# Kernel tuning notes

Measured on AMD Instinct MI355X. Metric: run time of the kernel, lower is better.

Reference implementation:

```python
import jax, jax.numpy as jnp
import numpy as np

WINDOW_3D = (5, 11, 11)
SIGMA_3D = (0.7, 1.5, 1.5)
VALUE_MAGNITUDE = 1.0
USE_GAUSSIAN = True
CHANNEL = 1


def _gaussian(n, sigma):
    x = np.arange(n, dtype=np.float64)
    g = np.exp(-((x - n // 2) ** 2) / (2.0 * sigma ** 2))
    return g / g.sum()


def _make_window():
    if USE_GAUSSIAN:
        wz = _gaussian(WINDOW_3D[0], SIGMA_3D[0])
        wy = _gaussian(WINDOW_3D[1], SIGMA_3D[1])
        wx = _gaussian(WINDOW_3D[2], SIGMA_3D[2])
    else:
        wz = np.full(WINDOW_3D[0], 1.0 / WINDOW_3D[0])
        wy = np.full(WINDOW_3D[1], 1.0 / WINDOW_3D[1])
        wx = np.full(WINDOW_3D[2], 1.0 / WINDOW_3D[2])
    win = np.einsum('z,y,x->zyx', wz, wy, wx).astype(np.float32)
    # depthwise kernel: (C, 1, wz, wy, wx)
    return jnp.asarray(np.broadcast_to(win, (CHANNEL, 1) + WINDOW_3D).copy())


def _dwconv3d(x, w):
    pad = [(s // 2, s // 2) for s in WINDOW_3D]
    return jax.lax.conv_general_dilated(
        x, w, window_strides=(1, 1, 1), padding=pad,
        dimension_numbers=('NCDHW', 'OIDHW', 'NCDHW'),
        feature_group_count=CHANNEL)


def setup_inputs() -> dict:
    key = jax.random.key(0)
    k1, k2 = jax.random.split(key)
    shape = (8, 1, 32, 256, 256)
    img1 = jax.random.uniform(k1, shape, dtype=jnp.float32)
    img2 = jax.random.uniform(k2, shape, dtype=jnp.float32)
    return {"img1": img1, "img2": img2}


def reference(img1, img2):
    w = _make_window().astype(img1.dtype)
    mu1 = _dwconv3d(img1, w)
    mu2 = _dwconv3d(img2, w)
    mu1_sq = mu1 * mu1
    mu2_sq = mu2 * mu2
    mu1_mu2 = mu1 * mu2
    sigma1_sq = _dwconv3d(img1 * img1, w) - mu1_sq
    sigma2_sq = _dwconv3d(img2 * img2, w) - mu2_sq
    sigma12 = _dwconv3d(img1 * img2, w) - mu1_mu2
    C1 = (VALUE_MAGNITUDE * 0.01) ** 2
    C2 = (VALUE_MAGNITUDE * 0.03) ** 2
    ssim_map = ((2 * mu1_mu2 + C1) * (2 * sigma12 + C2)) / (
        (mu1_sq + mu2_sq + C1) * (sigma1_sq + sigma2_sq + C2))
    ssim = jnp.mean(ssim_map, axis=(0, 2, 3, 4))  # per-channel mean
    return 1.0 - ssim
```

## Files before the change

kernel.cpp:

```cpp
#include <hip/hip_runtime.h>
#include <hip/hip_fp16.h>
#include <math.h>


typedef __attribute__((ext_vector_type(2))) float f32x2;

#define DEPTH   32
#define HEIGHT  256
#define WIDTH   256
#define HW      (HEIGHT*WIDTH)
#define COUNT   16777216.0
#define NACC    64

#define PDW   22
#define PROWS 44
#define PLSZ  (PROWS*PDW)

struct Weights { float wz[5]; float wy[11]; };

__device__ __forceinline__ f32x2 fma2(f32x2 a, f32x2 b, f32x2 c) {
  return __builtin_elementwise_fma(a, b, c);
}
__device__ __forceinline__ f32x2 bc2(float v) { f32x2 r; r.x = v; r.y = v; return r; }

__global__ __launch_bounds__(256, 4) void ssim3d_h16b(
    const float* __restrict__ img1, const float* __restrict__ img2,
    double* __restrict__ acc, Weights W)
{
  __shared__ __align__(16) __half2 PL[5 * PLSZ];
  __shared__ float wred[4];
  const int tid = threadIdx.x;

  int bid = blockIdx.x;
  bid = (bid & 7) * 2048 + (bid >> 3);
  const int txi = bid & 7, tyi = (bid >> 3) & 7, z_out = (bid >> 6) & 31, n = bid >> 11;
  const int x0 = txi * 32 - 6;
  const int y0 = tyi * 32 - 5;

  const int cp = tid % 22, g = tid / 22;
  f32x2 zacc[4][5];
#pragma unroll
  for (int i = 0; i < 4; ++i)
#pragma unroll
    for (int f = 0; f < 5; ++f) zacc[i][f] = bc2(0.f);

  if (g < 11) {
    const int gx0 = x0 + 2 * cp;
    if ((unsigned)gx0 <= 254u) {
      const size_t nbase = (size_t)n * DEPTH * HW;
      int rofs[4];
#pragma unroll
      for (int i = 0; i < 4; ++i) {
        int gy = y0 + 4 * g + i;
        rofs[i] = min(max(gy, 0), 255) * WIDTH;
      }
#pragma unroll
      for (int kz = 0; kz < 5; ++kz) {
        int z_in = z_out + kz - 2;
        if ((unsigned)z_in >= 32u) continue;
        const f32x2 wz2 = bc2(W.wz[kz]);
        const float* p1 = img1 + nbase + (size_t)z_in * HW + gx0;
        const float* p2 = img2 + nbase + (size_t)z_in * HW + gx0;
#pragma unroll
        for (int i = 0; i < 4; ++i) {
          f32x2 A = *(const f32x2*)(p1 + rofs[i]);
          f32x2 B = *(const f32x2*)(p2 + rofs[i]);
          f32x2 t = wz2 * A, u = wz2 * B;
          zacc[i][0] += t;
          zacc[i][1] += u;
          zacc[i][2] = fma2(t, A, zacc[i][2]);
          zacc[i][3] = fma2(u, B, zacc[i][3]);
          zacc[i][4] = fma2(t, B, zacc[i][4]);
        }
      }
    }
#pragma unroll
    for (int i = 0; i < 4; ++i) {
      int row = 4 * g + i;
#pragma unroll
      for (int f = 0; f < 5; ++f)
        PL[f * PLSZ + row * PDW + cp] =
            __float22half2_rn(make_float2(zacc[i][f].x, zacc[i][f].y));
    }
  }
  __syncthreads();

  __half2 wy2[11];
#pragma unroll
  for (int j = 0; j < 11; ++j) wy2[j] = __float2half2_rn(W.wy[j]);

  const int g2 = tid / 22, xp = tid % 22;
  const bool act3 = (g2 < 11);
  const bool yedge = (tyi == 0) || (tyi == 7);
#pragma unroll
  for (int f = 0; f < 5; ++f) {
    __half2 yout[3];
    if (act3) {
      const __half2* pf = PL + f * PLSZ + xp;
      __half2 win[13];
#pragma unroll
      for (int i = 0; i < 13; ++i) win[i] = pf[(3 * g2 + i) * PDW];
      if (yedge) {
#pragma unroll
        for (int i = 0; i < 13; ++i)
          if ((unsigned)(y0 + 3 * g2 + i) >= 256u) win[i] = __float2half2_rn(0.f);
      }
#pragma unroll
      for (int r = 0; r < 3; ++r) {
        __half2 s = __float2half2_rn(0.f);
#pragma unroll
        for (int j = 0; j < 11; ++j) s = __hfma2(wy2[j], win[r + j], s);
        yout[r] = s;
      }
    }
    __syncthreads();
    if (act3) {
#pragma unroll
      for (int r = 0; r < 3; ++r) {
        int y = 3 * g2 + r;
        if (y < 32) PL[f * PLSZ + y * PDW + xp] = yout[r];
      }
    }
  }
  __syncthreads();

  const int yy = tid & 31;
  const int xh = tid >> 5;
  float sf[5][4];
#pragma unroll
  for (int f = 0; f < 5; ++f) {
    const uint2* pp = (const uint2*)(PL + f * PLSZ + yy * PDW + xh * 2);
    uint2 d0 = pp[0], d1 = pp[1], d2 = pp[2], d3 = pp[3];
    unsigned dw[8] = {d0.x, d0.y, d1.x, d1.y, d2.x, d2.y, d3.x, d3.y};
    float w[16];
#pragma unroll
    for (int m = 0; m < 8; ++m) {
      float2 fp = __half22float2(*(__half2*)&dw[m]);
      w[2 * m] = fp.x; w[2 * m + 1] = fp.y;
    }
#pragma unroll
    for (int k = 0; k < 4; ++k) {
      float sv = 0.f;
#pragma unroll
      for (int j = 0; j < 11; ++j)
        sv = fmaf(W.wy[j], w[k + 1 + j], sv);
      sf[f][k] = sv;
    }
  }

  float lsum = 0.f;
  const float C1 = 1e-4f, C2 = 9e-4f;
#pragma unroll
  for (int k = 0; k < 4; ++k) {
    float mu1 = sf[0][k], mu2 = sf[1][k];
    float m11 = mu1 * mu1, m22 = mu2 * mu2, m12 = mu1 * mu2;
    float s1 = sf[2][k] - m11, s2 = sf[3][k] - m22, s12 = sf[4][k] - m12;
    float num = fmaf(2.f, m12, C1) * fmaf(2.f, s12, C2);
    float den = (m11 + m22 + C1) * (s1 + s2 + C2);
#if __has_builtin(__builtin_amdgcn_rcpf)
    lsum = fmaf(num, __builtin_amdgcn_rcpf(den), lsum);
#else
    lsum += num / den;
#endif
  }

#pragma unroll
  for (int off = 32; off > 0; off >>= 1) lsum += __shfl_down(lsum, off, 64);
  if ((tid & 63) == 0) wred[tid >> 6] = lsum;
  __syncthreads();
  if (tid == 0) {
    float bs = wred[0] + wred[1] + wred[2] + wred[3];
    atomicAdd(&acc[blockIdx.x & (NACC - 1)], (double)bs);
  }
}

__global__ void ssim3d_finalize(const double* __restrict__ acc, float* __restrict__ out)
{
  double s = 0.0;
  for (int i = 0; i < NACC; ++i) s += acc[i];
  out[0] = 1.0f - (float)(s / COUNT);
}

static Weights make_weights()
{
  Weights W;
  double gbuf[11]; double s;

  s = 0.0;
  for (int i = 0; i < 5; ++i) {
    double d = i - 2;
    gbuf[i] = exp(-(d * d) / (2.0 * 0.7 * 0.7));
    s += gbuf[i];
  }
  for (int i = 0; i < 5; ++i) W.wz[i] = (float)(gbuf[i] / s);

  s = 0.0;
  for (int i = 0; i < 11; ++i) {
    double d = i - 5;
    gbuf[i] = exp(-(d * d) / (2.0 * 1.5 * 1.5));
    s += gbuf[i];
  }
  for (int i = 0; i < 11; ++i) W.wy[i] = (float)(gbuf[i] / s);

  return W;
}

extern "C" void kernel_launch(void* const* d_in, const int* in_sizes, int n_in,
                              void* d_out, int out_size, void* d_ws, size_t ws_size,
                              hipStream_t stream)
{
  const float* img1 = (const float*)d_in[0];
  const float* img2 = (const float*)d_in[1];
  float* out = (float*)d_out;
  double* acc = (double*)d_ws;

  hipMemsetAsync(d_ws, 0, NACC * sizeof(double), stream);

  Weights W = make_weights();

  const int n_blocks = 8 * DEPTH * 8 * 8;
  ssim3d_h16b<<<dim3(n_blocks), dim3(256), 0, stream>>>(img1, img2, acc, W);
  ssim3d_finalize<<<1, 1, 0, stream>>>(acc, out);
}
```

Baseline: 131.4 us.

## Move z-pass and final x-pass to packed fp16 with compile-time weights

Converts inputs to fp16 right after loading and runs the z-direction accumulation with packed half FMAs instead of fp32. The final horizontal pass uses pair-packed fp16 weights, applying packed FMAs over the half2 data and summing the two lanes. Weights become compile-time constants, and launch bounds move from 4 to 6 blocks per SM for more occupancy. Doing more of the pipeline in fp16 cuts ALU work and register use, but raises rounding error, notably in the variance terms computed from squared half values.

```diff
diff --git a/kernel.cpp b/kernel.cpp
--- a/kernel.cpp
+++ b/kernel.cpp
@@ -1,9 +1,8 @@
 #include <hip/hip_runtime.h>
-#include <hip/hip_fp16.h>
-#include <math.h>
 
 
 typedef __attribute__((ext_vector_type(2))) float f32x2;
+typedef _Float16 h2 __attribute__((ext_vector_type(2)));
 
 #define DEPTH   32
 #define HEIGHT  256
@@ -13,23 +12,49 @@
 #define NACC    64
 
 #define PDW   22
-#define PROWS 44
-#define PLSZ  (PROWS*PDW)
-
-struct Weights { float wz[5]; float wy[11]; };
-
-__device__ __forceinline__ f32x2 fma2(f32x2 a, f32x2 b, f32x2 c) {
+#define PLSZ  (44*PDW)
+
+#define W0h 0x1436u
+#define W1h 0x1FC8u
+#define W2h 0x289Cu
+#define W3h 0x2F00u
+#define W4h 0x32D1u
+#define W5h 0x3442u
+
+__device__ __forceinline__ h2 h2bits(unsigned u) {
+  h2 r; __builtin_memcpy(&r, &u, 4); return r;
+}
+__device__ __forceinline__ h2 hfma2v(h2 a, h2 b, h2 c) {
   return __builtin_elementwise_fma(a, b, c);
 }
-__device__ __forceinline__ f32x2 bc2(float v) { f32x2 r; r.x = v; r.y = v; return r; }
-
-__global__ __launch_bounds__(256, 4) void ssim3d_h16b(
+__device__ __forceinline__ h2 pkrtz(float x, float y) {
+#if __has_builtin(__builtin_amdgcn_cvt_pkrtz)
+  auto t = __builtin_amdgcn_cvt_pkrtz(x, y);
+  h2 r; __builtin_memcpy(&r, &t, 4); return r;
+#else
+  h2 r; r.x = (_Float16)x; r.y = (_Float16)y; return r;
+#endif
+}
+
+__global__ __launch_bounds__(256, 6) void ssim3d_h16c(
     const float* __restrict__ img1, const float* __restrict__ img2,
-    double* __restrict__ acc, Weights W)
+    double* __restrict__ acc)
 {
-  __shared__ __align__(16) __half2 PL[5 * PLSZ];
+  __shared__ __align__(16) h2 PL[5 * PLSZ];
   __shared__ float wred[4];
   const int tid = threadIdx.x;
+
+  constexpr unsigned WYB[11] = {
+    W0h|(W0h<<16), W1h|(W1h<<16), W2h|(W2h<<16), W3h|(W3h<<16), W4h|(W4h<<16),
+    W5h|(W5h<<16),
+    W4h|(W4h<<16), W3h|(W3h<<16), W2h|(W2h<<16), W1h|(W1h<<16), W0h|(W0h<<16)};
+  constexpr unsigned WZB[5] = {
+    0x20ED20EDu, 0x32933293u, 0x388F388Fu, 0x32933293u, 0x20ED20EDu};
+  constexpr unsigned WP[4][8] = {
+    {0x14360000u, 0x289C1FC8u, 0x32D12F00u, 0x32D13442u, 0x289C2F00u, 0x14361FC8u, 0u, 0u},
+    {0u, 0x1FC81436u, 0x2F00289Cu, 0x344232D1u, 0x2F0032D1u, 0x1FC8289Cu, 0x00001436u, 0u},
+    {0u, 0x14360000u, 0x289C1FC8u, 0x32D12F00u, 0x32D13442u, 0x289C2F00u, 0x14361FC8u, 0u},
+    {0u, 0u, 0x1FC81436u, 0x2F00289Cu, 0x344232D1u, 0x2F0032D1u, 0x1FC8289Cu, 0x00001436u}};
 
   int bid = blockIdx.x;
   bid = (bid & 7) * 2048 + (bid >> 3);
@@ -38,11 +63,11 @@
   const int y0 = tyi * 32 - 5;
 
   const int cp = tid % 22, g = tid / 22;
-  f32x2 zacc[4][5];
+  h2 zacc[4][5];
 #pragma unroll
   for (int i = 0; i < 4; ++i)
 #pragma unroll
-    for (int f = 0; f < 5; ++f) zacc[i][f] = bc2(0.f);
+    for (int f = 0; f < 5; ++f) zacc[i][f] = (h2){(_Float16)0, (_Float16)0};
 
   if (g < 11) {
     const int gx0 = x0 + 2 * cp;
@@ -58,19 +83,19 @@
       for (int kz = 0; kz < 5; ++kz) {
         int z_in = z_out + kz - 2;
         if ((unsigned)z_in >= 32u) continue;
-        const f32x2 wz2 = bc2(W.wz[kz]);
+        const h2 wzh = h2bits(WZB[kz]);
         const float* p1 = img1 + nbase + (size_t)z_in * HW + gx0;
         const float* p2 = img2 + nbase + (size_t)z_in * HW + gx0;
 #pragma unroll
         for (int i = 0; i < 4; ++i) {
           f32x2 A = *(const f32x2*)(p1 + rofs[i]);
           f32x2 B = *(const f32x2*)(p2 + rofs[i]);
-          f32x2 t = wz2 * A, u = wz2 * B;
-          zacc[i][0] += t;
-          zacc[i][1] += u;
-          zacc[i][2] = fma2(t, A, zacc[i][2]);
-          zacc[i][3] = fma2(u, B, zacc[i][3]);
-          zacc[i][4] = fma2(t, B, zacc[i][4]);
+          h2 ah = pkrtz(A.x, A.y), bh = pkrtz(B.x, B.y);
+          zacc[i][0] = hfma2v(wzh, ah, zacc[i][0]);
+          zacc[i][1] = hfma2v(wzh, bh, zacc[i][1]);
+          zacc[i][2] = hfma2v(wzh, ah * ah, zacc[i][2]);
+          zacc[i][3] = hfma2v(wzh, bh * bh, zacc[i][3]);
+          zacc[i][4] = hfma2v(wzh, ah * bh, zacc[i][4]);
         }
       }
     }
@@ -79,37 +104,33 @@
       int row = 4 * g + i;
 #pragma unroll
       for (int f = 0; f < 5; ++f)
-        PL[f * PLSZ + row * PDW + cp] =
-            __float22half2_rn(make_float2(zacc[i][f].x, zacc[i][f].y));
+        PL[f * PLSZ + row * PDW + cp] = zacc[i][f];
     }
   }
   __syncthreads();
-
-  __half2 wy2[11];
-#pragma unroll
-  for (int j = 0; j < 11; ++j) wy2[j] = __float2half2_rn(W.wy[j]);
 
   const int g2 = tid / 22, xp = tid % 22;
   const bool act3 = (g2 < 11);
   const bool yedge = (tyi == 0) || (tyi == 7);
 #pragma unroll
   for (int f = 0; f < 5; ++f) {
-    __half2 yout[3];
+    h2 yout[3];
     if (act3) {
-      const __half2* pf = PL + f * PLSZ + xp;
-      __half2 win[13];
+      const h2* pf = PL + f * PLSZ + xp;
+      h2 win[13];
 #pragma unroll
       for (int i = 0; i < 13; ++i) win[i] = pf[(3 * g2 + i) * PDW];
       if (yedge) {
 #pragma unroll
         for (int i = 0; i < 13; ++i)
-          if ((unsigned)(y0 + 3 * g2 + i) >= 256u) win[i] = __float2half2_rn(0.f);
+          if ((unsigned)(y0 + 3 * g2 + i) >= 256u)
+            win[i] = (h2){(_Float16)0, (_Float16)0};
       }
 #pragma unroll
       for (int r = 0; r < 3; ++r) {
-        __half2 s = __float2half2_rn(0.f);
-#pragma unroll
-        for (int j = 0; j < 11; ++j) s = __hfma2(wy2[j], win[r + j], s);
+        h2 s = (h2){(_Float16)0, (_Float16)0};
+#pragma unroll
+        for (int j = 0; j < 11; ++j) s = hfma2v(h2bits(WYB[j]), win[r + j], s);
         yout[r] = s;
       }
     }
@@ -129,22 +150,17 @@
   float sf[5][4];
 #pragma unroll
   for (int f = 0; f < 5; ++f) {
-    const uint2* pp = (const uint2*)(PL + f * PLSZ + yy * PDW + xh * 2);
-    uint2 d0 = pp[0], d1 = pp[1], d2 = pp[2], d3 = pp[3];
-    unsigned dw[8] = {d0.x, d0.y, d1.x, d1.y, d2.x, d2.y, d3.x, d3.y};
-    float w[16];
-#pragma unroll
-    for (int m = 0; m < 8; ++m) {
-      float2 fp = __half22float2(*(__half2*)&dw[m]);
-      w[2 * m] = fp.x; w[2 * m + 1] = fp.y;
-    }
+    const h2* pp = PL + f * PLSZ + yy * PDW + xh * 2;
+    h2 d[8];
+#pragma unroll
+    for (int m = 0; m < 8; ++m) d[m] = pp[m];
 #pragma unroll
     for (int k = 0; k < 4; ++k) {
-      float sv = 0.f;
-#pragma unroll
-      for (int j = 0; j < 11; ++j)
-        sv = fmaf(W.wy[j], w[k + 1 + j], sv);
-      sf[f][k] = sv;
+      h2 a = (h2){(_Float16)0, (_Float16)0};
+#pragma unroll
+      for (int m = 0; m < 8; ++m)
+        if (WP[k][m]) a = hfma2v(h2bits(WP[k][m]), d[m], a);
+      sf[f][k] = (float)a.x + (float)a.y;
     }
   }
 
@@ -181,30 +197,6 @@
   out[0] = 1.0f - (float)(s / COUNT);
 }
 
-static Weights make_weights()
-{
-  Weights W;
-  double gbuf[11]; double s;
-
-  s = 0.0;
-  for (int i = 0; i < 5; ++i) {
-    double d = i - 2;
-    gbuf[i] = exp(-(d * d) / (2.0 * 0.7 * 0.7));
-    s += gbuf[i];
-  }
-  for (int i = 0; i < 5; ++i) W.wz[i] = (float)(gbuf[i] / s);
-
-  s = 0.0;
-  for (int i = 0; i < 11; ++i) {
-    double d = i - 5;
-    gbuf[i] = exp(-(d * d) / (2.0 * 1.5 * 1.5));
-    s += gbuf[i];
-  }
-  for (int i = 0; i < 11; ++i) W.wy[i] = (float)(gbuf[i] / s);
-
-  return W;
-}
-
 extern "C" void kernel_launch(void* const* d_in, const int* in_sizes, int n_in,
                               void* d_out, int out_size, void* d_ws, size_t ws_size,
                               hipStream_t stream)
@@ -214,11 +206,9 @@
   float* out = (float*)d_out;
   double* acc = (double*)d_ws;
 
-  hipMemsetAsync(d_ws, 0, NACC * sizeof(double), stream);
-
-  Weights W = make_weights();
+  (void)hipMemsetAsync(d_ws, 0, NACC * sizeof(double), stream);
 
   const int n_blocks = 8 * DEPTH * 8 * 8;
-  ssim3d_h16b<<<dim3(n_blocks), dim3(256), 0, stream>>>(img1, img2, acc, W);
+  ssim3d_h16c<<<dim3(n_blocks), dim3(256), 0, stream>>>(img1, img2, acc);
   ssim3d_finalize<<<1, 1, 0, stream>>>(acc, out);
 }
```

Measured after the change: 115.3 us. 1.14x faster.
